# Kernel tuning notes

Measured on AMD Instinct MI355X. Metric: run time of the kernel, lower is better.

## Reference

```python
import jax, jax.numpy as jnp
import numpy as np

N_NODES = 25000
N_EDGES = 100000
NODE_IN = 8
EDGE_IN = 4
HID = 32


def _glorot(key, shape):
    fan_in, fan_out = shape[0], shape[-1]
    s = jnp.sqrt(2.0 / (fan_in + fan_out))
    return jax.random.normal(key, shape, dtype=jnp.float32) * s


def setup_inputs() -> dict:
    key = jax.random.key(0)
    ks = jax.random.split(key, 16)
    x = jax.random.normal(ks[0], (N_NODES, NODE_IN), dtype=jnp.float32)
    edge_index = jax.random.randint(ks[1], (2, N_EDGES), 0, N_NODES, dtype=jnp.int64)
    edge_attr = jax.random.uniform(ks[2], (N_EDGES, EDGE_IN), dtype=jnp.float32)
    params = {
        # conv1: edge MLP (edge_in -> node_in*hid), root lin (node_in->hid, no bias), bias
        'w_mlp1': _glorot(ks[3], (EDGE_IN, NODE_IN * HID)),
        'b_mlp1': jnp.zeros((NODE_IN * HID,), jnp.float32),
        'root1': _glorot(ks[4], (NODE_IN, HID)),
        'bias1': jnp.zeros((HID,), jnp.float32),
        # conv2
        'w_mlp2': _glorot(ks[5], (EDGE_IN, HID * HID)),
        'b_mlp2': jnp.zeros((HID * HID,), jnp.float32),
        'root2': _glorot(ks[6], (HID, HID)),
        'bias2': jnp.zeros((HID,), jnp.float32),
        # conv3
        'w_mlp3': _glorot(ks[7], (EDGE_IN, HID * HID)),
        'b_mlp3': jnp.zeros((HID * HID,), jnp.float32),
        'root3': _glorot(ks[8], (HID, HID)),
        'bias3': jnp.zeros((HID,), jnp.float32),
        # output head: Linear(hid,hid) -> ReLU -> Linear(hid,1)
        'w_out1': _glorot(ks[9], (HID, HID)),
        'b_out1': jnp.zeros((HID,), jnp.float32),
        'w_out2': _glorot(ks[10], (HID, 1)),
        'b_out2': jnp.zeros((1,), jnp.float32),
    }
    return {'x': x, 'edge_index': edge_index, 'edge_attr': edge_attr, **params}


def _nnconv(x, src, dst, edge_attr, w_mlp, b_mlp, root, bias, in_dim, out_dim, num_nodes):
    # edge MLP -> per-edge weight matrix [E, in, out]
    w_e = jax.nn.relu(edge_attr @ w_mlp + b_mlp).reshape(-1, in_dim, out_dim)
    # gather source features, per-edge matvec
    msg = jnp.einsum('ei,eio->eo', x[src], w_e)  # [E, out]
    # scatter-mean into target nodes
    agg = jax.ops.segment_sum(msg, dst, num_segments=num_nodes)
    cnt = jax.ops.segment_sum(jnp.ones((msg.shape[0],), msg.dtype), dst, num_segments=num_nodes)
    agg = agg / jnp.maximum(cnt, 1.0)[:, None]
    return agg + x @ root + bias


def reference(x, edge_index, edge_attr,
              w_mlp1, b_mlp1, root1, bias1,
              w_mlp2, b_mlp2, root2, bias2,
              w_mlp3, b_mlp3, root3, bias3,
              w_out1, b_out1, w_out2, b_out2):
    src, dst = edge_index[0], edge_index[1]
    n = x.shape[0]
    h = jax.nn.relu(_nnconv(x, src, dst, edge_attr, w_mlp1, b_mlp1, root1, bias1, NODE_IN, HID, n))
    h = jax.nn.relu(_nnconv(h, src, dst, edge_attr, w_mlp2, b_mlp2, root2, bias2, HID, HID, n))
    h = jax.nn.relu(_nnconv(h, src, dst, edge_attr, w_mlp3, b_mlp3, root3, bias3, HID, HID, n))
    h = jax.nn.relu(h @ w_out1 + b_out1)
    return h @ w_out2 + b_out2  # [N, 1]
```

## Files before the change

kernel.cpp:

```cpp
#include <hip/hip_runtime.h>

#define HID 32
#define CAP 32

__global__ __launch_bounds__(256) void build_kernel(
    const int* __restrict__ src, const int* __restrict__ dst,
    const float* __restrict__ ea,
    int* __restrict__ deg, int* __restrict__ perm_src, float4* __restrict__ perm_ea,
    int E)
{
    int e = blockIdx.x * blockDim.x + threadIdx.x;
    if (e >= E) return;
    int d = dst[e];
    int pos = atomicAdd(deg + d, 1) & (CAP - 1);
    size_t slot = (size_t)d * CAP + pos;
    perm_src[slot] = src[e];
    perm_ea[slot]  = *(const float4*)(ea + (size_t)e * 4);
}

__device__ __forceinline__ float edge_quad(const float4 av, const float4 xv,
                                           const float4 WA, const float4 WB,
                                           const float4 WC, const float4 WD,
                                           const float4 BR, float acc)
{
    float t;
    t = fmaf(av.x, WA.x, BR.x); t = fmaf(av.y, WB.x, t); t = fmaf(av.z, WC.x, t); t = fmaf(av.w, WD.x, t);
    acc = fmaf(xv.x, fmaxf(t, 0.f), acc);
    t = fmaf(av.x, WA.y, BR.y); t = fmaf(av.y, WB.y, t); t = fmaf(av.z, WC.y, t); t = fmaf(av.w, WD.y, t);
    acc = fmaf(xv.y, fmaxf(t, 0.f), acc);
    t = fmaf(av.x, WA.z, BR.z); t = fmaf(av.y, WB.z, t); t = fmaf(av.z, WC.z, t); t = fmaf(av.w, WD.z, t);
    acc = fmaf(xv.z, fmaxf(t, 0.f), acc);
    t = fmaf(av.x, WA.w, BR.w); t = fmaf(av.y, WB.w, t); t = fmaf(av.z, WC.w, t); t = fmaf(av.w, WD.w, t);
    acc = fmaf(xv.w, fmaxf(t, 0.f), acc);
    return acc;
}

__global__ __launch_bounds__(256, 6) void pull8_kernel(
    const float* __restrict__ x,
    const int* __restrict__ deg,
    const int* __restrict__ perm_src, const float4* __restrict__ perm_ea,
    const float* __restrict__ w_mlp,
    const float* __restrict__ b_mlp,
    const float* __restrict__ root,
    const float* __restrict__ bias,
    float* __restrict__ h_out,
    int N)
{
    constexpr int IN = 8, NPG = 4;
    const int lane = threadIdx.x & 63;
    const int o = lane & 31, half = lane >> 5;
    const int wave = (blockIdx.x * blockDim.x + threadIdx.x) >> 6;
    const int v0 = wave * NPG;
    if (v0 >= N) return;

    const int cb = half * 4 * HID + o;
    const float4 WA = make_float4(w_mlp[cb],       w_mlp[cb+32],       w_mlp[cb+64],       w_mlp[cb+96]);
    const float4 WB = make_float4(w_mlp[256+cb],   w_mlp[256+cb+32],   w_mlp[256+cb+64],   w_mlp[256+cb+96]);
    const float4 WC = make_float4(w_mlp[512+cb],   w_mlp[512+cb+32],   w_mlp[512+cb+64],   w_mlp[512+cb+96]);
    const float4 WD = make_float4(w_mlp[768+cb],   w_mlp[768+cb+32],   w_mlp[768+cb+64],   w_mlp[768+cb+96]);
    const float4 BR = make_float4(b_mlp[cb],       b_mlp[cb+32],       b_mlp[cb+64],       b_mlp[cb+96]);
    const float4 RO = make_float4(root[cb],        root[cb+32],        root[cb+64],        root[cb+96]);
    const float bo = bias[o];

    for (int nv = 0; nv < NPG; ++nv) {
        const int v = v0 + nv;
        if (v >= N) break;
        const int dt = deg[v];
        const int dg = min(dt, CAP);
        const int* ps = perm_src + (size_t)v * CAP;
        const float4* pe = perm_ea + (size_t)v * CAP;

        float acc = 0.f;
        for (int k0 = 0; k0 < dg; k0 += 4) {
            int4 s4 = *(const int4*)(ps + k0);
            const int ss[4] = { s4.x, s4.y, s4.z, s4.w };
            float4 aa[4];
            #pragma unroll
            for (int j = 0; j < 4; ++j) aa[j] = pe[k0 + j];
            float4 xg[4];
            #pragma unroll
            for (int j = 0; j < 4; ++j)
                xg[j] = *(const float4*)(x + (size_t)ss[j] * IN + half * 4);
            #pragma unroll
            for (int j = 0; j < 4; ++j)
                if (k0 + j < dg)
                    acc = edge_quad(aa[j], xg[j], WA, WB, WC, WD, BR, acc);
        }
        const float4 xr = *(const float4*)(x + (size_t)v * IN + half * 4);
        float rpart = fmaf(xr.x, RO.x, fmaf(xr.y, RO.y, fmaf(xr.z, RO.z, xr.w * RO.w)));
        float part = acc / fmaxf((float)dt, 1.f) + rpart;
        part += __shfl_down(part, 32);
        if (lane < 32)
            h_out[(size_t)v * HID + o] = fmaxf(part + bo, 0.f);
    }
}

template<bool HEAD>
__global__ __launch_bounds__(256) __attribute__((amdgpu_waves_per_eu(2, 2)))
void pull32_kernel(
    const float* __restrict__ h_in,
    const int* __restrict__ deg,
    const int* __restrict__ perm_src, const float4* __restrict__ perm_ea,
    const float* __restrict__ w_mlp,
    const float* __restrict__ b_mlp,
    const float* __restrict__ root,
    const float* __restrict__ bias,
    const float* __restrict__ hw1, const float* __restrict__ hb1,
    const float* __restrict__ hw2, const float* __restrict__ hb2,
    float* __restrict__ h_out,
    int N)
{
    constexpr int IN = 32, NPW = 8;
    const int lane = threadIdx.x & 63;
    const int o = lane & 31, half = lane >> 5;
    const int wave = (blockIdx.x * blockDim.x + threadIdx.x) >> 6;
    const int v0 = wave * NPW;
    if (v0 >= N) return;
    const int vEnd = min(v0 + NPW, N);
    const int hoff = half << 4;

    float4 WA[4], WB[4], WC[4], WD[4], BR[4], RO[4];
    #pragma unroll
    for (int k = 0; k < 4; ++k) {
        const int ib = (hoff + (k << 2)) * HID + o;
        WA[k] = make_float4(w_mlp[ib],      w_mlp[ib+32],      w_mlp[ib+64],      w_mlp[ib+96]);
        WB[k] = make_float4(w_mlp[1024+ib], w_mlp[1024+ib+32], w_mlp[1024+ib+64], w_mlp[1024+ib+96]);
        WC[k] = make_float4(w_mlp[2048+ib], w_mlp[2048+ib+32], w_mlp[2048+ib+64], w_mlp[2048+ib+96]);
        WD[k] = make_float4(w_mlp[3072+ib], w_mlp[3072+ib+32], w_mlp[3072+ib+64], w_mlp[3072+ib+96]);
        BR[k] = make_float4(b_mlp[ib],      b_mlp[ib+32],      b_mlp[ib+64],      b_mlp[ib+96]);
        RO[k] = make_float4(root[ib],       root[ib+32],       root[ib+64],       root[ib+96]);
    }
    const float bo = bias[o];

    int vC = v0, k0C = 0;
    int dgC = deg[v0];
    float4 aC0 = perm_ea[(size_t)v0 * CAP];
    float4 aC1 = perm_ea[(size_t)v0 * CAP + 1];
    float4 xC0[4], xC1[4];
    {
        const int2 s2 = *(const int2*)(perm_src + (size_t)v0 * CAP);
        const float* p0 = h_in + (size_t)s2.x * IN + hoff;
        const float* p1 = h_in + (size_t)s2.y * IN + hoff;
        #pragma unroll
        for (int q = 0; q < 4; ++q) { xC0[q] = *(const float4*)(p0 + 4*q); xC1[q] = *(const float4*)(p1 + 4*q); }
    }
    float acc = 0.f;

    #pragma unroll 2
    for (;;) {
        const int dgCc = min(dgC, CAP);
        const bool lastB = (k0C + 2 >= dgCc);
        const int vN  = lastB ? vC + 1 : vC;
        const int k0N = lastB ? 0 : k0C + 2;
        const bool haveN = (vN < vEnd);

        int dgN = 0;
        float4 aN0, aN1, xN0[4], xN1[4];
        if (haveN) {
            dgN = deg[vN];
            const int2 s2N = *(const int2*)(perm_src + (size_t)vN * CAP + k0N);
            aN0 = perm_ea[(size_t)vN * CAP + k0N];
            aN1 = perm_ea[(size_t)vN * CAP + k0N + 1];
            const float* p0 = h_in + (size_t)s2N.x * IN + hoff;
            const float* p1 = h_in + (size_t)s2N.y * IN + hoff;
            #pragma unroll
            for (int q = 0; q < 4; ++q) { xN0[q] = *(const float4*)(p0 + 4*q); xN1[q] = *(const float4*)(p1 + 4*q); }
        }

        float4 rC[4];
        if (lastB) {
            const float* rp = h_in + (size_t)vC * IN + hoff;
            #pragma unroll
            for (int q = 0; q < 4; ++q) rC[q] = *(const float4*)(rp + 4*q);
        }

        if (k0C < dgCc) {
            #pragma unroll
            for (int k = 0; k < 4; ++k)
                acc = edge_quad(aC0, xC0[k], WA[k], WB[k], WC[k], WD[k], BR[k], acc);
        }
        if (k0C + 1 < dgCc) {
            #pragma unroll
            for (int k = 0; k < 4; ++k)
                acc = edge_quad(aC1, xC1[k], WA[k], WB[k], WC[k], WD[k], BR[k], acc);
        }

        if (lastB) {
            float rpart = 0.f;
            #pragma unroll
            for (int k = 0; k < 4; ++k) {
                rpart = fmaf(rC[k].x, RO[k].x, rpart);
                rpart = fmaf(rC[k].y, RO[k].y, rpart);
                rpart = fmaf(rC[k].z, RO[k].z, rpart);
                rpart = fmaf(rC[k].w, RO[k].w, rpart);
            }
            float part = acc / fmaxf((float)dgC, 1.f) + rpart;
            part += __shfl_down(part, 32);
            if (lane < 32) {
                float h = fmaxf(part + bo, 0.f);
                if (!HEAD) {
                    h_out[(size_t)vC * HID + o] = h;
                } else {
                    float tt = hb1[o];
                    #pragma unroll
                    for (int i = 0; i < HID; ++i)
                        tt = fmaf(__shfl(h, i, 32), hw1[i * HID + o], tt);
                    tt = fmaxf(tt, 0.f) * hw2[o];
                    #pragma unroll
                    for (int dd = 16; dd > 0; dd >>= 1)
                        tt += __shfl_down(tt, dd, 32);
                    if (o == 0) h_out[vC] = tt + hb2[0];
                }
            }
            acc = 0.f;
        }

        if (!haveN) break;
        vC = vN; k0C = k0N; dgC = dgN;
        aC0 = aN0; aC1 = aN1;
        #pragma unroll
        for (int q = 0; q < 4; ++q) { xC0[q] = xN0[q]; xC1[q] = xN1[q]; }
    }
}

extern "C" void kernel_launch(void* const* d_in, const int* in_sizes, int n_in,
                              void* d_out, int out_size, void* d_ws, size_t ws_size,
                              hipStream_t stream)
{
    const float* x      = (const float*)d_in[0];
    const int*   ei     = (const int*)d_in[1];
    const float* ea     = (const float*)d_in[2];
    const float* w_mlp1 = (const float*)d_in[3];
    const float* b_mlp1 = (const float*)d_in[4];
    const float* root1  = (const float*)d_in[5];
    const float* bias1  = (const float*)d_in[6];
    const float* w_mlp2 = (const float*)d_in[7];
    const float* b_mlp2 = (const float*)d_in[8];
    const float* root2  = (const float*)d_in[9];
    const float* bias2  = (const float*)d_in[10];
    const float* w_mlp3 = (const float*)d_in[11];
    const float* b_mlp3 = (const float*)d_in[12];
    const float* root3  = (const float*)d_in[13];
    const float* bias3  = (const float*)d_in[14];
    const float* w_out1 = (const float*)d_in[15];
    const float* b_out1 = (const float*)d_in[16];
    const float* w_out2 = (const float*)d_in[17];
    const float* b_out2 = (const float*)d_in[18];

    const int NODE_IN = 8;
    const int N = in_sizes[0] / NODE_IN;
    const int E = in_sizes[2] / 4;
    const int* src = ei;
    const int* dst = ei + E;

    char* ws = (char*)d_ws;
    size_t off = 0;
    auto carve = [&](size_t bytes) {
        char* p = ws + off;
        off += (bytes + 255) & ~(size_t)255;
        return p;
    };
    int*    deg      = (int*)carve((size_t)N * 4);
    int*    perm_src = (int*)carve((size_t)N * CAP * 4);
    float4* perm_ea  = (float4*)carve((size_t)N * CAP * 16);
    float*  h1       = (float*)carve((size_t)N * HID * 4);
    float*  h2       = (float*)carve((size_t)N * HID * 4);
    float*  outp     = (float*)d_out;
    size_t zero_bytes = (size_t)((char*)perm_src - (char*)deg) + (size_t)N * CAP * 4;

    const int TB = 256;
    const int buildBlocks = (E + TB - 1) / TB;
    const int p8Blocks  = (N + 4 * 4 - 1) / (4 * 4);
    const int p32Blocks = (N + 8 * 4 - 1) / (8 * 4);

    hipMemsetAsync(deg, 0, zero_bytes, stream);

    build_kernel<<<buildBlocks, TB, 0, stream>>>(src, dst, ea, deg, perm_src, perm_ea, E);

    pull8_kernel<<<p8Blocks, TB, 0, stream>>>(x, deg, perm_src, perm_ea,
                                              w_mlp1, b_mlp1, root1, bias1, h1, N);

    pull32_kernel<false><<<p32Blocks, TB, 0, stream>>>(h1, deg, perm_src, perm_ea,
                                                       w_mlp2, b_mlp2, root2, bias2,
                                                       nullptr, nullptr, nullptr, nullptr, h2, N);

    pull32_kernel<true><<<p32Blocks, TB, 0, stream>>>(h2, deg, perm_src, perm_ea,
                                                      w_mlp3, b_mlp3, root3, bias3,
                                                      w_out1, b_out1, w_out2, b_out2, outp, N);
}
```

Baseline: 238.5 us.

## Restructure conv32 loop to process one node per iteration with 4-edge batches

Replaces the 2-edge software-pipelined loop that could straddle node boundaries with a per-node loop. Each iteration handles the first 4 edges in one unrolled block, prefetching the next node's first two gathers, and any remaining edges in batches of 4 with all gathers issued together. Root weights are reloaded from memory per node instead of held in registers, and empty asm statements pin the MLP weights in VGPRs. The aim is more memory-level parallelism per wave and lower register pressure, at the cost of extra root loads and wasted gathers for nodes with fewer than 4 edges.

Result: slower. 249.5 us (+4.6%).

```diff
diff --git a/kernel.cpp b/kernel.cpp
--- a/kernel.cpp
+++ b/kernel.cpp
@@ -119,7 +119,7 @@
     const int vEnd = min(v0 + NPW, N);
     const int hoff = half << 4;
 
-    float4 WA[4], WB[4], WC[4], WD[4], BR[4], RO[4];
+    float4 WA[4], WB[4], WC[4], WD[4], BR[4];
     #pragma unroll
     for (int k = 0; k < 4; ++k) {
         const int ib = (hoff + (k << 2)) * HID + o;
@@ -128,98 +128,135 @@
         WC[k] = make_float4(w_mlp[2048+ib], w_mlp[2048+ib+32], w_mlp[2048+ib+64], w_mlp[2048+ib+96]);
         WD[k] = make_float4(w_mlp[3072+ib], w_mlp[3072+ib+32], w_mlp[3072+ib+64], w_mlp[3072+ib+96]);
         BR[k] = make_float4(b_mlp[ib],      b_mlp[ib+32],      b_mlp[ib+64],      b_mlp[ib+96]);
-        RO[k] = make_float4(root[ib],       root[ib+32],       root[ib+64],       root[ib+96]);
+    }
+    #pragma unroll
+    for (int k = 0; k < 4; ++k) {
+        asm volatile("" : "+v"(WA[k].x), "+v"(WA[k].y), "+v"(WA[k].z), "+v"(WA[k].w));
+        asm volatile("" : "+v"(WB[k].x), "+v"(WB[k].y), "+v"(WB[k].z), "+v"(WB[k].w));
+        asm volatile("" : "+v"(WC[k].x), "+v"(WC[k].y), "+v"(WC[k].z), "+v"(WC[k].w));
+        asm volatile("" : "+v"(WD[k].x), "+v"(WD[k].y), "+v"(WD[k].z), "+v"(WD[k].w));
+        asm volatile("" : "+v"(BR[k].x), "+v"(BR[k].y), "+v"(BR[k].z), "+v"(BR[k].w));
     }
     const float bo = bias[o];
 
-    int vC = v0, k0C = 0;
     int dgC = deg[v0];
-    float4 aC0 = perm_ea[(size_t)v0 * CAP];
-    float4 aC1 = perm_ea[(size_t)v0 * CAP + 1];
-    float4 xC0[4], xC1[4];
+    int s2C, s3C;
+    float4 aaC[4], xg0[4], xg1[4];
     {
-        const int2 s2 = *(const int2*)(perm_src + (size_t)v0 * CAP);
-        const float* p0 = h_in + (size_t)s2.x * IN + hoff;
-        const float* p1 = h_in + (size_t)s2.y * IN + hoff;
-        #pragma unroll
-        for (int q = 0; q < 4; ++q) { xC0[q] = *(const float4*)(p0 + 4*q); xC1[q] = *(const float4*)(p1 + 4*q); }
-    }
-    float acc = 0.f;
-
-    #pragma unroll 2
-    for (;;) {
-        const int dgCc = min(dgC, CAP);
-        const bool lastB = (k0C + 2 >= dgCc);
-        const int vN  = lastB ? vC + 1 : vC;
-        const int k0N = lastB ? 0 : k0C + 2;
+        int4 s4 = *(const int4*)(perm_src + (size_t)v0 * CAP);
+        s2C = s4.z; s3C = s4.w;
+        #pragma unroll
+        for (int j = 0; j < 4; ++j) aaC[j] = perm_ea[(size_t)v0 * CAP + j];
+        const float* p0 = h_in + (size_t)s4.x * IN + hoff;
+        const float* p1 = h_in + (size_t)s4.y * IN + hoff;
+        #pragma unroll
+        for (int q = 0; q < 4; ++q) { xg0[q] = *(const float4*)(p0 + 4*q); xg1[q] = *(const float4*)(p1 + 4*q); }
+    }
+
+    for (int nv = 0; nv < NPW; ++nv) {
+        const int v = v0 + nv;
+        if (v >= vEnd) break;
+        const int dgc = min(dgC, CAP);
+
+        float4 xg2[4], xg3[4];
+        {
+            const float* p2 = h_in + (size_t)s2C * IN + hoff;
+            const float* p3 = h_in + (size_t)s3C * IN + hoff;
+            #pragma unroll
+            for (int q = 0; q < 4; ++q) { xg2[q] = *(const float4*)(p2 + 4*q); xg3[q] = *(const float4*)(p3 + 4*q); }
+        }
+        float4 rC[4];
+        {
+            const float* rp = h_in + (size_t)v * IN + hoff;
+            #pragma unroll
+            for (int q = 0; q < 4; ++q) rC[q] = *(const float4*)(rp + 4*q);
+        }
+        const int vN = v + 1;
         const bool haveN = (vN < vEnd);
-
-        int dgN = 0;
-        float4 aN0, aN1, xN0[4], xN1[4];
+        int dgN = 0, s2N = 0, s3N = 0;
+        float4 aaN[4], xn0[4], xn1[4];
         if (haveN) {
             dgN = deg[vN];
-            const int2 s2N = *(const int2*)(perm_src + (size_t)vN * CAP + k0N);
-            aN0 = perm_ea[(size_t)vN * CAP + k0N];
-            aN1 = perm_ea[(size_t)vN * CAP + k0N + 1];
-            const float* p0 = h_in + (size_t)s2N.x * IN + hoff;
-            const float* p1 = h_in + (size_t)s2N.y * IN + hoff;
-            #pragma unroll
-            for (int q = 0; q < 4; ++q) { xN0[q] = *(const float4*)(p0 + 4*q); xN1[q] = *(const float4*)(p1 + 4*q); }
-        }
-
-        float4 rC[4];
-        if (lastB) {
-            const float* rp = h_in + (size_t)vC * IN + hoff;
-            #pragma unroll
-            for (int q = 0; q < 4; ++q) rC[q] = *(const float4*)(rp + 4*q);
-        }
-
-        if (k0C < dgCc) {
-            #pragma unroll
-            for (int k = 0; k < 4; ++k)
-                acc = edge_quad(aC0, xC0[k], WA[k], WB[k], WC[k], WD[k], BR[k], acc);
-        }
-        if (k0C + 1 < dgCc) {
-            #pragma unroll
-            for (int k = 0; k < 4; ++k)
-                acc = edge_quad(aC1, xC1[k], WA[k], WB[k], WC[k], WD[k], BR[k], acc);
-        }
-
-        if (lastB) {
-            float rpart = 0.f;
-            #pragma unroll
-            for (int k = 0; k < 4; ++k) {
-                rpart = fmaf(rC[k].x, RO[k].x, rpart);
-                rpart = fmaf(rC[k].y, RO[k].y, rpart);
-                rpart = fmaf(rC[k].z, RO[k].z, rpart);
-                rpart = fmaf(rC[k].w, RO[k].w, rpart);
-            }
-            float part = acc / fmaxf((float)dgC, 1.f) + rpart;
-            part += __shfl_down(part, 32);
-            if (lane < 32) {
-                float h = fmaxf(part + bo, 0.f);
-                if (!HEAD) {
-                    h_out[(size_t)vC * HID + o] = h;
-                } else {
-                    float tt = hb1[o];
-                    #pragma unroll
-                    for (int i = 0; i < HID; ++i)
-                        tt = fmaf(__shfl(h, i, 32), hw1[i * HID + o], tt);
-                    tt = fmaxf(tt, 0.f) * hw2[o];
-                    #pragma unroll
-                    for (int dd = 16; dd > 0; dd >>= 1)
-                        tt += __shfl_down(tt, dd, 32);
-                    if (o == 0) h_out[vC] = tt + hb2[0];
+            int4 s4 = *(const int4*)(perm_src + (size_t)vN * CAP);
+            s2N = s4.z; s3N = s4.w;
+            #pragma unroll
+            for (int j = 0; j < 4; ++j) aaN[j] = perm_ea[(size_t)vN * CAP + j];
+            const float* p0 = h_in + (size_t)s4.x * IN + hoff;
+            const float* p1 = h_in + (size_t)s4.y * IN + hoff;
+            #pragma unroll
+            for (int q = 0; q < 4; ++q) { xn0[q] = *(const float4*)(p0 + 4*q); xn1[q] = *(const float4*)(p1 + 4*q); }
+        }
+
+        float acc = 0.f;
+        #pragma unroll
+        for (int j = 0; j < 4; ++j) {
+            if (j < dgc) {
+                #pragma unroll
+                for (int k = 0; k < 4; ++k) {
+                    const float4 xv = (j == 0) ? xg0[k] : (j == 1) ? xg1[k] : (j == 2) ? xg2[k] : xg3[k];
+                    acc = edge_quad(aaC[j], xv, WA[k], WB[k], WC[k], WD[k], BR[k], acc);
                 }
             }
-            acc = 0.f;
-        }
-
-        if (!haveN) break;
-        vC = vN; k0C = k0N; dgC = dgN;
-        aC0 = aN0; aC1 = aN1;
-        #pragma unroll
-        for (int q = 0; q < 4; ++q) { xC0[q] = xN0[q]; xC1[q] = xN1[q]; }
+        }
+
+        for (int k0 = 4; k0 < dgc; k0 += 4) {
+            const int* ps = perm_src + (size_t)v * CAP + k0;
+            const float4* pe = perm_ea + (size_t)v * CAP + k0;
+            int4 s4 = *(const int4*)(ps);
+            const int st[4] = { s4.x, s4.y, s4.z, s4.w };
+            float4 at[4], xt[4][4];
+            #pragma unroll
+            for (int j = 0; j < 4; ++j) at[j] = pe[j];
+            #pragma unroll
+            for (int j = 0; j < 4; ++j) {
+                const float* xp = h_in + (size_t)st[j] * IN + hoff;
+                #pragma unroll
+                for (int q = 0; q < 4; ++q) xt[j][q] = *(const float4*)(xp + 4*q);
+            }
+            #pragma unroll
+            for (int j = 0; j < 4; ++j) {
+                if (k0 + j < dgc) {
+                    #pragma unroll
+                    for (int k = 0; k < 4; ++k)
+                        acc = edge_quad(at[j], xt[j][k], WA[k], WB[k], WC[k], WD[k], BR[k], acc);
+                }
+            }
+        }
+
+        float rpart = 0.f;
+        #pragma unroll
+        for (int k = 0; k < 4; ++k) {
+            const int ib = (hoff + (k << 2)) * HID + o;
+            const float4 RO = make_float4(root[ib], root[ib+32], root[ib+64], root[ib+96]);
+            rpart = fmaf(rC[k].x, RO.x, rpart);
+            rpart = fmaf(rC[k].y, RO.y, rpart);
+            rpart = fmaf(rC[k].z, RO.z, rpart);
+            rpart = fmaf(rC[k].w, RO.w, rpart);
+        }
+        float part = acc / fmaxf((float)dgC, 1.f) + rpart;
+        part += __shfl_down(part, 32);
+        if (lane < 32) {
+            float h = fmaxf(part + bo, 0.f);
+            if (!HEAD) {
+                h_out[(size_t)v * HID + o] = h;
+            } else {
+                float tt = hb1[o];
+                #pragma unroll
+                for (int i = 0; i < HID; ++i)
+                    tt = fmaf(__shfl(h, i, 32), hw1[i * HID + o], tt);
+                tt = fmaxf(tt, 0.f) * hw2[o];
+                #pragma unroll
+                for (int dd = 16; dd > 0; dd >>= 1)
+                    tt += __shfl_down(tt, dd, 32);
+                if (o == 0) h_out[v] = tt + hb2[0];
+            }
+        }
+
+        dgC = dgN; s2C = s2N; s3C = s3N;
+        #pragma unroll
+        for (int j = 0; j < 4; ++j) aaC[j] = aaN[j];
+        #pragma unroll
+        for (int q = 0; q < 4; ++q) { xg0[q] = xn0[q]; xg1[q] = xn1[q]; }
     }
 }
 
```
